# Kernel optimization log

Measured on AMD Instinct MI355X. Metric: run time of the kernel, lower is better.

## Reference

```python
import jax, jax.numpy as jnp
import numpy as np

N, E, D, ED, K = 16384, 524288, 64, 64, 16


def _lrelu(x, s):
    return jnp.where(x >= 0, x, s * x)


def _bn(x, g, b):
    # BatchNorm1d in training mode: biased batch statistics, eps=1e-5
    m = jnp.mean(x, axis=0)
    v = jnp.var(x, axis=0)
    return g * (x - m) * jax.lax.rsqrt(v + 1e-5) + b


def _segmax(msg, dst, n):
    # PyG aggr='max'; empty segments -> 0
    out = jax.ops.segment_max(msg, dst, num_segments=n)
    return jnp.where(jnp.isneginf(out), 0.0, out)


def _knn(x, k):
    # cosine kNN with self loops (bt_cosine=True, bt_self_loop=True)
    n = x.shape[0]
    xn = x * jax.lax.rsqrt(jnp.sum(x * x, axis=1, keepdims=True) + 1e-12)
    sim = jnp.where(jnp.eye(n, dtype=bool), -jnp.inf, xn @ xn.T)  # [n,n]
    idx = jax.lax.top_k(sim, k)[1]  # [n,k] sources j per target i
    loops = jnp.arange(n)
    src = jnp.concatenate([idx.reshape(-1), loops])
    dst = jnp.concatenate([jnp.repeat(loops, k), loops])
    return src, dst


def _static(x, src, dst, ea, w1, w2, w3, wl, n):
    # message: cat(x_j - x_i, edge_attr); scatter-max; update MLP (LeakyReLU 0.1)
    msg = jnp.concatenate([x[src] - x[dst], ea], axis=1)
    h = _segmax(msg, dst, n)
    h = _lrelu(h @ w1, 0.1)
    h = _lrelu(h @ w2, 0.1)
    h = _lrelu(h @ w3, 0.1)
    return _lrelu(x @ wl, 0.1) + h


def _dynamic(x, k, m1, m2, wl, n):
    # kNN recomputed under no_grad each call
    src, dst = _knn(jax.lax.stop_gradient(x), k)
    xi = x[dst]
    m = jnp.concatenate([xi, x[src] - xi], axis=1)
    m = _lrelu(m @ m1, 0.2)
    m = _lrelu(m @ m2, 0.2)
    return _lrelu(x @ wl, 0.1) + _segmax(m, dst, n)


def setup_inputs() -> dict:
    key = jax.random.key(0)
    ks = jax.random.split(key, 32)
    def w(i, shape):
        return jax.random.normal(ks[i], shape, dtype=jnp.float32) * 0.05
    return {
        'node_embedding': w(0, (N, D)),
        'edge_embedding': w(1, (E, ED)),
        'edge_index': jax.random.randint(ks[2], (2, E), 0, N),
        'k': K,
        'sg1_w1': w(3, (128, 96)), 'sg1_w2': w(4, (96, 64)), 'sg1_w3': w(5, (64, 64)), 'sg1_lin': w(6, (64, 64)),
        'sg2_w1': w(7, (128, 128)), 'sg2_w2': w(8, (128, 128)), 'sg2_w3': w(9, (128, 128)), 'sg2_lin': w(10, (64, 128)),
        'sg3_w1': w(11, (192, 192)), 'sg3_w2': w(12, (192, 192)), 'sg3_w3': w(13, (192, 192)), 'sg3_lin': w(14, (128, 192)),
        'dg1_m1': w(15, (128, 128)), 'dg1_m2': w(16, (128, 128)), 'dg1_lin': w(17, (64, 128)),
        'dg2_m1': w(18, (256, 192)), 'dg2_m2': w(19, (192, 192)), 'dg2_lin': w(20, (128, 192)),
        'f1_w': w(21, (704, 1024)), 'f1_g': jnp.ones(1024, jnp.float32), 'f1_b': jnp.zeros(1024, jnp.float32),
        'f2_w1': w(22, (1728, 512)), 'f2_g1': jnp.ones(512, jnp.float32), 'f2_b1': jnp.zeros(512, jnp.float32),
        'f2_w2': w(23, (512, 256)), 'f2_g2': jnp.ones(256, jnp.float32), 'f2_b2': jnp.zeros(256, jnp.float32),
        'f2_w3': w(24, (256, 128)),
    }


def reference(node_embedding, edge_embedding, edge_index, k,
              sg1_w1, sg1_w2, sg1_w3, sg1_lin,
              sg2_w1, sg2_w2, sg2_w3, sg2_lin,
              sg3_w1, sg3_w2, sg3_w3, sg3_lin,
              dg1_m1, dg1_m2, dg1_lin,
              dg2_m1, dg2_m2, dg2_lin,
              f1_w, f1_g, f1_b,
              f2_w1, f2_g1, f2_b1, f2_w2, f2_g2, f2_b2, f2_w3):
    n = node_embedding.shape[0]
    src, dst = edge_index[0], edge_index[1]
    sg1 = _static(node_embedding, src, dst, edge_embedding, sg1_w1, sg1_w2, sg1_w3, sg1_lin, n)
    sg2 = _static(sg1, src, dst, edge_embedding, sg2_w1, sg2_w2, sg2_w3, sg2_lin, n)
    sg3 = _static(sg2, src, dst, edge_embedding, sg3_w1, sg3_w2, sg3_w3, sg3_lin, n)
    dg1 = _dynamic(sg1, k, dg1_m1, dg1_m2, dg1_lin, n)
    dg2 = _dynamic(dg1, k, dg2_m1, dg2_m2, dg2_lin, n)
    cat1 = jnp.concatenate([sg1, dg1, dg2, sg2, sg3], axis=1)  # [N, 704]
    f1 = _lrelu(_bn(cat1 @ f1_w, f1_g, f1_b), 0.2)
    cat2 = jnp.concatenate([f1, cat1], axis=1)  # [N, 1728]
    h = _lrelu(_bn(cat2 @ f2_w1, f2_g1, f2_b1), 0.2)
    h = _lrelu(_bn(h @ f2_w2, f2_g2, f2_b2), 0.2)
    return h @ f2_w3  # [N, 128]
```

## Files before the change

### kernel.cpp

```cpp
#include <hip/hip_runtime.h>
#include <math.h>

typedef unsigned short u16;
typedef unsigned int u32;
typedef unsigned long long u64;
typedef __attribute__((ext_vector_type(8))) short short8v;
typedef __attribute__((ext_vector_type(4))) float f32x4;

static const int NN  = 16384;
static const int NE  = 524288;
static const int SCC = 1024;
static const int KEDGE = 17;

__device__ __forceinline__ u16 f2b(float v){
  u32 u = __float_as_uint(v);
  u += 0x7FFFu + ((u >> 16) & 1u);
  return (u16)(u >> 16);
}
__device__ __forceinline__ float b2f(u16 h){ return __uint_as_float(((u32)h) << 16); }

__device__ __forceinline__ void gl_lds16(const u16* g, u16* l){
  __builtin_amdgcn_global_load_lds(
      (const __attribute__((address_space(1))) u32*)(g),
      (__attribute__((address_space(3))) u32*)(l), 16, 0, 0);
}

__global__ void k_fill_i32(int* p, int v, int n){
  int i = blockIdx.x*256 + threadIdx.x; if (i < n) p[i] = v;
}
__global__ void k_split3(const float* __restrict__ s, u16* __restrict__ h,
                         u16* __restrict__ m, u16* __restrict__ l, int n,
                         int C, int ldo, int co, int ldl){
  int i = blockIdx.x*256 + threadIdx.x; if (i >= n) return;
  int r = i / C, c = i % C;
  float v = s[i];
  u16 hh = f2b(v);
  float rr = v - b2f(hh);
  u16 mm_ = f2b(rr);
  size_t o = (size_t)r*ldo + co + c;
  h[o] = hh; m[o] = mm_;
  if (l) l[(size_t)r*ldl + c] = f2b(rr - b2f(mm_));
}
__global__ void k_wprep3(const float* __restrict__ W, int K, int N, int Npad,
                         u16* __restrict__ h, u16* __restrict__ m, u16* __restrict__ l){
  int idx = blockIdx.x*256 + threadIdx.x; if (idx >= K*Npad) return;
  int n = idx / K, k = idx % K;
  float v = (n < N) ? W[(size_t)k*N + n] : 0.f;
  u16 hh = f2b(v); h[idx] = hh;
  float r = v - b2f(hh);
  u16 mm_ = f2b(r); m[idx] = mm_;
  l[idx] = f2b(r - b2f(mm_));
}

__global__ void k_hist(const int* __restrict__ dst, int* __restrict__ cnt){
  int e = blockIdx.x*256 + threadIdx.x; if (e < NE) atomicAdd(&cnt[dst[e]], 1);
}
__global__ void k_scan(const int* __restrict__ cnt, int* __restrict__ off){
  __shared__ int part[1024];
  int t = threadIdx.x;
  int base = t*16;
  int loc[16]; int s = 0;
#pragma unroll
  for (int q=0;q<16;q++){ loc[q] = s; s += cnt[base+q]; }
  part[t] = s; __syncthreads();
  for (int d=1; d<1024; d<<=1){
    int v = (t>=d) ? part[t-d] : 0; __syncthreads();
    part[t] += v; __syncthreads();
  }
  int prev = (t==0) ? 0 : part[t-1];
#pragma unroll
  for (int q=0;q<16;q++) off[base+q] = prev + loc[q];
  if (t == 1023) off[NN] = part[1023];
}
__global__ void k_csr_fill(const int* __restrict__ src, const int* __restrict__ dst,
                           const int* __restrict__ off, int* __restrict__ cur,
                           int* __restrict__ csrc, int* __restrict__ ceid){
  int e = blockIdx.x*256 + threadIdx.x; if (e >= NE) return;
  int d = dst[e];
  int p = atomicAdd(&cur[d], 1);
  int idx = off[d] + p;
  csrc[idx] = src[e];
  ceid[idx] = e;
}

__global__ void k_static_segmax(const float* __restrict__ x, int Dx,
                                const float* __restrict__ ea,
                                const int* __restrict__ off,
                                const int* __restrict__ csrc,
                                const int* __restrict__ ceid,
                                u16* __restrict__ th, u16* __restrict__ tm,
                                u16* __restrict__ tl){
  int i = blockIdx.x, c = threadIdx.x;
  int DM = Dx + 64;
  int s = off[i], e = off[i+1];
  float mx = -INFINITY;
  float v;
  if (c < Dx){
    for (int t = s; t < e; t++) mx = fmaxf(mx, x[(size_t)csrc[t]*Dx + c]);
    v = (s == e) ? 0.f : (mx - x[(size_t)i*Dx + c]);
  } else {
    int cc = c - Dx;
    for (int t = s; t < e; t++) mx = fmaxf(mx, ea[(size_t)ceid[t]*64 + cc]);
    v = (s == e) ? 0.f : mx;
  }
  size_t o = (size_t)i*DM + c;
  u16 h = f2b(v); th[o] = h;
  float r = v - b2f(h);
  u16 mm_ = f2b(r); tm[o] = mm_;
  tl[o] = f2b(r - b2f(mm_));
}

template<int P, int GATHER>
__global__ __launch_bounds__(256) void k_mgemm(
    const u16* __restrict__ Ah, const u16* __restrict__ Am, const u16* __restrict__ Al,
    int lda, int ldal,
    const u16* __restrict__ Bh, const u16* __restrict__ Bm, const u16* __restrict__ Bl,
    int ldb,
    float* __restrict__ Cf, u16* __restrict__ Ch, u16* __restrict__ Cm, u16* __restrict__ Cl,
    int ldc, int ldsp, int cosp, int ldspl,
    int K, int Nc, float slope, int flags, int colbase,
    const float* __restrict__ Xf, const int* __restrict__ topig, int c0g, int Dxg)
{
  constexpr int NC = (P == 3) ? 3 : 2;
  __shared__ u16 lds[NC*2*4096];
  const int t = threadIdx.x;
  const int m0 = blockIdx.y * 128, n0 = blockIdx.x * 128;
  const int wave = t >> 6, lane = t & 63;
  const int wr = (wave >> 1) << 6, wc = (wave & 1) << 6;
  const int l15 = lane & 15, l4 = lane >> 4;
  f32x4 acc[4][4] = {};

  const u16* Ap[3] = {Ah, Am, Al};
  const int ldav[3] = {lda, lda, ldal};
  const u16* Bp[3] = {Bh, Bm, Bl};

  const int c0c = wave*128 + lane, c1c = c0c + 64;
  const int r0c = c0c & 127, s0c = c0c >> 7;
  const int r1c = c1c & 127, s1c = c1c >> 7;
  const int lb0 = (wave*128)*8;
  const int lb1 = (wave*128 + 64)*8;

  size_t gA0[3], gA1[3], gB0[3], gB1[3];
#pragma unroll
  for (int cc=0; cc<NC; cc++){
    if (!GATHER){
      gA0[cc] = (size_t)(m0 + r0c)*ldav[cc] + s0c*8;
      gA1[cc] = (size_t)(m0 + r1c)*ldav[cc] + s1c*8;
    }
    gB0[cc] = (size_t)(n0 + r0c)*ldb + s0c*8;
    gB1[cc] = (size_t)(n0 + r1c)*ldb + s1c*8;
  }

  const int sr = t & 127, sseg = t >> 7;
  int node_i = 0, node_j = 0;
  if (GATHER){
    int erow = m0 + sr;
    int i = c0g + erow / KEDGE;
    int slot = erow % KEDGE;
    node_i = i;
    node_j = (slot < 16) ? topig[i*16 + slot] : i;
  }

  for (int k0 = 0; k0 < K; k0 += 32){
    __attribute__((aligned(16))) u16 hb[16], mb[16], lcb[16];
    if (GATHER){
      int kpos = k0 + sseg*16;
      bool side = kpos < Dxg;
      int kk = side ? kpos : kpos - Dxg;
      const float* xi = Xf + (size_t)node_i*Dxg + kk;
      const float* xj = Xf + (size_t)node_j*Dxg + kk;
#pragma unroll
      for (int q4=0;q4<4;q4++){
        float4 a = *(const float4*)(xi + q4*4);
        if (!side){
          float4 b = *(const float4*)(xj + q4*4);
          a = make_float4(b.x-a.x, b.y-a.y, b.z-a.z, b.w-a.w);
        }
        float vv[4] = {a.x, a.y, a.z, a.w};
#pragma unroll
        for (int q=0;q<4;q++){
          float v = vv[q];
          u16 h = f2b(v); hb[q4*4+q] = h;
          float r = v - b2f(h);
          u16 mm_ = f2b(r); mb[q4*4+q] = mm_;
          if (NC == 3) lcb[q4*4+q] = f2b(r - b2f(mm_));
        }
      }
    }
    __syncthreads();
    if (GATHER){
      int base0 = (sseg*2)*1024 + sr*8;
      int base1 = (sseg*2+1)*1024 + sr*8;
      *(int4*)&lds[0*4096 + base0] = *(const int4*)&hb[0];
      *(int4*)&lds[0*4096 + base1] = *(const int4*)&hb[8];
      *(int4*)&lds[1*4096 + base0] = *(const int4*)&mb[0];
      *(int4*)&lds[1*4096 + base1] = *(const int4*)&mb[8];
      if (NC == 3){
        *(int4*)&lds[2*4096 + base0] = *(const int4*)&lcb[0];
        *(int4*)&lds[2*4096 + base1] = *(const int4*)&lcb[8];
      }
    } else {
#pragma unroll
      for (int cc=0; cc<NC; cc++){
        gl_lds16(Ap[cc] + gA0[cc] + k0, &lds[cc*4096 + lb0]);
        gl_lds16(Ap[cc] + gA1[cc] + k0, &lds[cc*4096 + lb1]);
      }
    }
#pragma unroll
    for (int cc=0; cc<NC; cc++){
      gl_lds16(Bp[cc] + gB0[cc] + k0, &lds[(NC+cc)*4096 + lb0]);
      gl_lds16(Bp[cc] + gB1[cc] + k0, &lds[(NC+cc)*4096 + lb1]);
    }
    __syncthreads();
    short8v fa[NC][4], fb[NC][4];
#pragma unroll
    for (int m=0;m<4;m++){
      int ra = l4*1024 + (wr + m*16 + l15)*8;
      int rb = l4*1024 + (wc + m*16 + l15)*8;
#pragma unroll
      for (int cc=0;cc<NC;cc++){
        fa[cc][m] = *(const short8v*)&lds[cc*4096 + ra];
        fb[cc][m] = *(const short8v*)&lds[(NC+cc)*4096 + rb];
      }
    }
#pragma unroll
    for (int m=0;m<4;m++)
#pragma unroll
      for (int n=0;n<4;n++){
        if (P == 3){
          acc[m][n] = __builtin_amdgcn_mfma_f32_16x16x32_bf16(fa[1][m], fb[1][n], acc[m][n], 0,0,0);
          acc[m][n] = __builtin_amdgcn_mfma_f32_16x16x32_bf16(fa[0][m], fb[2][n], acc[m][n], 0,0,0);
          acc[m][n] = __builtin_amdgcn_mfma_f32_16x16x32_bf16(fa[2][m], fb[0][n], acc[m][n], 0,0,0);
        }
        acc[m][n] = __builtin_amdgcn_mfma_f32_16x16x32_bf16(fa[0][m], fb[1][n], acc[m][n], 0,0,0);
        acc[m][n] = __builtin_amdgcn_mfma_f32_16x16x32_bf16(fa[1][m], fb[0][n], acc[m][n], 0,0,0);
        acc[m][n] = __builtin_amdgcn_mfma_f32_16x16x32_bf16(fa[0][m], fb[0][n], acc[m][n], 0,0,0);
      }
  }

  const float NEG = -__builtin_inff();
#pragma unroll
  for (int n=0;n<4;n++){
    int col0 = n0 + wc + n*16;
    if (col0 >= Nc) continue;
    int col = col0 + l15;
#pragma unroll
    for (int m=0;m<4;m++){
      int rowb = m0 + wr + m*16 + l4*4;
#pragma unroll
      for (int r=0;r<4;r++){
        int row = rowb + r;
        float v = acc[m][n][r];
        if ((flags & 2) && row == colbase + col) v = NEG;
        else v = (v >= 0.f) ? v : v*slope;
        if (col < Nc){
          if (flags & 1) v += Cf[(size_t)row*ldc + col];
          if (Cf) Cf[(size_t)row*ldc + col] = v;
          if (Ch){
            size_t o = (size_t)row*ldsp + cosp + col;
            u16 h = f2b(v); Ch[o] = h;
            float rr = v - b2f(h);
            u16 mm_ = f2b(rr); Cm[o] = mm_;
            if (Cl) Cl[(size_t)row*ldspl + col] = f2b(rr - b2f(mm_));
          }
        }
      }
    }
  }
}

__global__ void k_normalize(const float* __restrict__ x,
                            u16* __restrict__ oh, u16* __restrict__ om,
                            u16* __restrict__ ol, int Dx){
  int i = blockIdx.x, lane = threadIdx.x;
  size_t o0 = (size_t)i*Dx + lane;
  float a = x[o0];
  float b = 0.f;
  if (Dx == 128) b = x[o0 + 64];
  float ss = a*a + b*b;
  for (int d = 32; d; d >>= 1) ss += __shfl_xor(ss, d);
  float rs = rsqrtf(ss + 1e-12f);
  float va = a*rs;
  u16 h = f2b(va); oh[o0] = h;
  float r = va - b2f(h);
  u16 mm_ = f2b(r); om[o0] = mm_;
  ol[o0] = f2b(r - b2f(mm_));
  if (Dx == 128){
    float vb = b*rs;
    u16 h2 = f2b(vb); oh[o0+64] = h2;
    float r2 = vb - b2f(h2);
    u16 m2 = f2b(r2); om[o0+64] = m2;
    ol[o0+64] = f2b(r2 - b2f(m2));
  }
}

__global__ void k_topk_merge(const float* __restrict__ S, int colbase,
                             float* __restrict__ topv, int* __restrict__ topi,
                             int first){
  const float INF = __builtin_inff();
  int i = blockIdx.x*4 + (threadIdx.x >> 6);
  int lane = threadIdx.x & 63;
  const float* row = S + (size_t)i * SCC;

  float4 va = *(const float4*)(row + 0*256 + lane*4);
  float4 vb = *(const float4*)(row + 1*256 + lane*4);
  float4 vc = *(const float4*)(row + 2*256 + lane*4);
  float4 vd = *(const float4*)(row + 3*256 + lane*4);
  float cv[16]; int cj[16];
  {
    float t0[4]={va.x,va.y,va.z,va.w}, t1[4]={vb.x,vb.y,vb.z,vb.w},
          t2[4]={vc.x,vc.y,vc.z,vc.w}, t3[4]={vd.x,vd.y,vd.z,vd.w};
#pragma unroll
    for (int q=0;q<4;q++){
      cv[q]    = t0[q]; cj[q]    = colbase + 0*256 + lane*4 + q;
      cv[4+q]  = t1[q]; cj[4+q]  = colbase + 1*256 + lane*4 + q;
      cv[8+q]  = t2[q]; cj[8+q]  = colbase + 2*256 + lane*4 + q;
      cv[12+q] = t3[q]; cj[12+q] = colbase + 3*256 + lane*4 + q;
    }
#pragma unroll
    for (int q=0;q<16;q++) if (cj[q] == i) cv[q] = -INF;
  }

  float pv = -INF; int pj = 0x7fffffff;
  if (!first){
    if (lane < 16){ pv = topv[i*16+lane]; pj = topi[i*16+lane]; }
    float tv = __shfl(pv, 15); int tj = __shfl(pj, 15);
    int cnt = 0;
#pragma unroll
    for (int q=0;q<16;q++){
      bool s = (cv[q] > tv) || (cv[q] == tv && cj[q] < tj);
      cnt += __popcll(__ballot(s));
    }
    if (cnt == 0) return;
    if (cnt <= 24){
#pragma unroll
      for (int q=0;q<16;q++){
        bool s = (cv[q] > tv) || (cv[q] == tv && cj[q] < tj);
        u64 msk = __ballot(s);
        while (msk){
          int src = __ffsll((long long)msk) - 1; msk &= msk - 1;
          float v = __shfl(cv[q], src);
          int   j = __shfl(cj[q], src);
          if ((v > tv) || (v == tv && j < tj)){
            bool eb = (pv > v) || (pv == v && pj < j);
            u32 mb = (u32)__ballot(eb) & 0xFFFFu;
            int p = __popc(mb);
            float sv = __shfl_up(pv, 1); int sj = __shfl_up(pj, 1);
            if (lane < 16 && lane >= p){
              if (lane == p){ pv = v; pj = j; }
              else          { pv = sv; pj = sj; }
            }
            tv = __shfl(pv, 15); tj = __shfl(pj, 15);
          }
        }
      }
      if (lane < 16){ topv[i*16+lane] = pv; topi[i*16+lane] = pj; }
      return;
    }
  }

  float myv = -INF; int myj = 0x7fffffff;
#pragma unroll
  for (int r=0;r<16;r++){
    float lv = pv; int lj = pj;
#pragma unroll
    for (int q=0;q<16;q++){
      if ((cv[q] > lv) || (cv[q] == lv && cj[q] < lj)){ lv = cv[q]; lj = cj[q]; }
    }
    float bv = lv; int bj = lj;
    for (int d=32; d; d>>=1){
      float ov = __shfl_xor(bv, d); int oj = __shfl_xor(bj, d);
      if ((ov > bv) || (ov == bv && oj < bj)){ bv = ov; bj = oj; }
    }
    if (lj == bj){
      if (pj == bj) pv = -INF;
      else {
#pragma unroll
        for (int q=0;q<16;q++) if (cj[q] == bj) cv[q] = -INF;
      }
    }
    if (lane == r){ myv = bv; myj = bj; }
  }
  if (lane < 16){ topv[i*16+lane] = myv; topi[i*16+lane] = myj; }
}

__global__ void k_segmax_add(const float* __restrict__ mo, int H2, int c0,
                             float* __restrict__ outp){
  int ii = blockIdx.x;
  int c = threadIdx.x;
  float m = -INFINITY;
  for (int s=0;s<KEDGE;s++) m = fmaxf(m, mo[(size_t)(ii*KEDGE+s)*H2 + c]);
  outp[(size_t)(c0+ii)*H2 + c] += m;
}

__global__ void k_bn_part(const float* __restrict__ X, int C,
                          float* __restrict__ psum, float* __restrict__ psq){
  int c = blockIdx.x*64 + (threadIdx.x & 63);
  int rl = threadIdx.x >> 6;
  int r0 = blockIdx.y * 512;
  float s = 0.f, q = 0.f;
  for (int r = r0 + rl; r < r0 + 512; r += 4){
    float v = X[(size_t)r*C + c];
    s += v; q += v*v;
  }
  __shared__ float ls[256], lq[256];
  ls[threadIdx.x] = s; lq[threadIdx.x] = q;
  __syncthreads();
  if (rl == 0){
    int tt = threadIdx.x;
    psum[blockIdx.y*C + c] = ls[tt] + ls[tt+64] + ls[tt+128] + ls[tt+192];
    psq [blockIdx.y*C + c] = lq[tt] + lq[tt+64] + lq[tt+128] + lq[tt+192];
  }
}
__global__ void k_bn_stats(const float* __restrict__ psum, const float* __restrict__ psq,
                           int C, float* __restrict__ stat){
  int c = blockIdx.x*256 + threadIdx.x; if (c >= C) return;
  float s = 0.f, q = 0.f;
  for (int ch=0; ch<32; ch++){ s += psum[ch*C + c]; q += psq[ch*C + c]; }
  float m = s * (1.f/16384.f);
  float var = q * (1.f/16384.f) - m*m;
  stat[c] = m;
  stat[C + c] = rsqrtf(var + 1e-5f);
}
__global__ void k_bn_apply(const float* __restrict__ X, int Cshift, int C,
                           const float* __restrict__ stat,
                           const float* __restrict__ g, const float* __restrict__ b,
                           u16* __restrict__ Oh, u16* __restrict__ Om,
                           int ldo, int co, int total){
  for (int idx = blockIdx.x*256 + threadIdx.x; idx < total; idx += gridDim.x*256){
    int c = idx & (C-1);
    int r = idx >> Cshift;
    float v = (X[idx] - stat[c]) * stat[C + c] * g[c] + b[c];
    v = (v >= 0.f) ? v : 0.2f*v;
    size_t o = (size_t)r*ldo + co + c;
    u16 h = f2b(v); Oh[o] = h;
    Om[o] = f2b(v - b2f(h));
  }
}

extern "C" void kernel_launch(void* const* d_in, const int* in_sizes, int n_in,
                              void* d_out, int out_size, void* d_ws, size_t ws_size,
                              hipStream_t stream) {
  (void)in_sizes; (void)n_in; (void)out_size; (void)ws_size;
  const float* x0   = (const float*)d_in[0];
  const float* ea   = (const float*)d_in[1];
  const int*   ei   = (const int*)d_in[2];
  const float* f1_g = (const float*)d_in[23];
  const float* f1_b = (const float*)d_in[24];
  const float* f2_g1= (const float*)d_in[26];
  const float* f2_b1= (const float*)d_in[27];
  const float* f2_g2= (const float*)d_in[29];
  const float* f2_b2= (const float*)d_in[30];
  float* out = (float*)d_out;

  const float* wsrc[22] = {
    (const float*)d_in[4],(const float*)d_in[5],(const float*)d_in[6],(const float*)d_in[7],
    (const float*)d_in[8],(const float*)d_in[9],(const float*)d_in[10],(const float*)d_in[11],
    (const float*)d_in[12],(const float*)d_in[13],(const float*)d_in[14],(const float*)d_in[15],
    (const float*)d_in[16],(const float*)d_in[17],(const float*)d_in[18],
    (const float*)d_in[19],(const float*)d_in[20],(const float*)d_in[21],
    (const float*)d_in[22],(const float*)d_in[25],(const float*)d_in[28],(const float*)d_in[31]
  };
  const int wK[22] = {128,96,64,64, 128,128,128,64, 192,192,192,128,
                      128,128,64, 256,192,128, 704, 1728, 512, 256};
  const int wN[22] = {96,64,64,64, 128,128,128,128, 192,192,192,192,
                      128,128,128, 192,192,192, 1024, 512, 256, 128};
  int wNp[22];
  for (int i=0;i<22;i++) wNp[i] = (wN[i] + 127) & ~127;

  char* w = (char*)d_ws;
  size_t off = 0;
  auto alloc = [&](size_t bytes)->char*{
    char* p = w + off; off = (off + bytes + 255) & ~(size_t)255; return p;
  };
  float* sg1f = (float*)alloc((size_t)NN*64*4);
  float* sg2f = (float*)alloc((size_t)NN*128*4);
  float* dg1f = (float*)alloc((size_t)NN*128*4);
  u16* cat1h = (u16*)alloc((size_t)NN*704*2);
  u16* cat1m = (u16*)alloc((size_t)NN*704*2);
  u16* sg1l  = (u16*)alloc((size_t)NN*64*2);
  u16* dg1l  = (u16*)alloc((size_t)NN*128*2);
  float* bnp  = (float*)alloc((size_t)2*32*1024*4);
  float* bns  = (float*)alloc((size_t)2*1024*4);
  u16 *wh[22], *wm[22], *wl[22];
  for (int i=0;i<22;i++){
    size_t e = (size_t)wK[i]*wNp[i];
    wh[i] = (u16*)alloc(e*2); wm[i] = (u16*)alloc(e*2); wl[i] = (u16*)alloc(e*2);
  }
  char* arena = alloc((size_t)120*1024*1024);
  size_t ac = 0;
  auto aalloc = [&](size_t b)->char*{
    char* p = arena + ac; ac = (ac + b + 255) & ~(size_t)255; return p;
  };

  auto MG = [&](int P, const u16* Ah, const u16* Am, const u16* Al, int lda, int ldal,
                const u16* Bh, const u16* Bm, const u16* Bl, int ldb,
                float* Cf, u16* Ch, u16* Cm, u16* Cl, int ldc, int ldsp, int cosp, int ldspl,
                int M, int K, int Nc, float slope, int flags, int colbase){
    dim3 g((Nc+127)/128, M/128);
    if (P == 3)
      k_mgemm<3,0><<<g,256,0,stream>>>(Ah,Am,Al,lda,ldal,Bh,Bm,Bl,ldb,
        Cf,Ch,Cm,Cl,ldc,ldsp,cosp,ldspl,K,Nc,slope,flags,colbase,nullptr,nullptr,0,0);
    else
      k_mgemm<2,0><<<g,256,0,stream>>>(Ah,Am,Al,lda,ldal,Bh,Bm,Bl,ldb,
        Cf,Ch,Cm,Cl,ldc,ldsp,cosp,ldspl,K,Nc,slope,flags,colbase,nullptr,nullptr,0,0);
  };
  auto MGG = [&](int P, const float* Xf, const int* topig, int c0g, int Dxg,
                 const u16* Bh, const u16* Bm, const u16* Bl, int ldb,
                 u16* Ch, u16* Cm, u16* Cl, int ldsp, int ldspl,
                 int M, int Nc, float slope){
    dim3 g((Nc+127)/128, M/128);
    if (P == 3)
      k_mgemm<3,1><<<g,256,0,stream>>>(nullptr,nullptr,nullptr,0,0,Bh,Bm,Bl,ldb,
        nullptr,Ch,Cm,Cl,0,ldsp,0,ldspl,2*Dxg,Nc,slope,0,0,Xf,topig,c0g,Dxg);
    else
      k_mgemm<2,1><<<g,256,0,stream>>>(nullptr,nullptr,nullptr,0,0,Bh,Bm,Bl,ldb,
        nullptr,Ch,Cm,Cl,0,ldsp,0,ldspl,2*Dxg,Nc,slope,0,0,Xf,topig,c0g,Dxg);
  };

  for (int i=0;i<22;i++){
    int e = wK[i]*wNp[i];
    k_wprep3<<<(e+255)/256, 256, 0, stream>>>(wsrc[i], wK[i], wN[i], wNp[i], wh[i], wm[i], wl[i]);
  }

  ac = 0;
  u16* t1s[3]; for (int c=0;c<3;c++) t1s[c] = (u16*)aalloc((size_t)NN*192*2);
  u16* t2s[3]; for (int c=0;c<3;c++) t2s[c] = (u16*)aalloc((size_t)NN*192*2);
  float* sof32 = (float*)aalloc((size_t)NN*192*4);
  int* csr_cnt = (int*)aalloc((size_t)NN*4);
  int* csr_off = (int*)aalloc((size_t)(NN+1)*4);
  int* csr_src = (int*)aalloc((size_t)NE*4);
  int* csr_eid = (int*)aalloc((size_t)NE*4);
  u16* x0s[3]; for (int c=0;c<3;c++) x0s[c] = (u16*)aalloc((size_t)NN*64*2);

  k_split3<<<(NN*64+255)/256, 256, 0, stream>>>(x0, x0s[0], x0s[1], x0s[2], NN*64, 64, 64, 0, 64);

  const int* srcp = ei;
  const int* dstp = ei + NE;
  k_fill_i32<<<(NN+255)/256, 256, 0, stream>>>(csr_cnt, 0, NN);
  k_hist<<<NE/256, 256, 0, stream>>>(dstp, csr_cnt);
  k_scan<<<1, 1024, 0, stream>>>(csr_cnt, csr_off);
  k_fill_i32<<<(NN+255)/256, 256, 0, stream>>>(csr_cnt, 0, NN);
  k_csr_fill<<<NE/256, 256, 0, stream>>>(srcp, dstp, csr_off, csr_cnt, csr_src, csr_eid);

  auto static_layer = [&](int P, const float* xf,
                          const u16* xh, const u16* xm, const u16* xl, int lda, int ldal,
                          int Dx, int wi, float* of, int co, u16* lout, int H1, int H2){
    int DM = Dx + 64;
    k_static_segmax<<<NN, DM, 0, stream>>>(xf, Dx, ea, csr_off, csr_src, csr_eid,
                                           t1s[0], t1s[1], t1s[2]);
    MG(P, t1s[0],t1s[1],t1s[2], DM,DM, wh[wi],wm[wi],wl[wi], DM,
       nullptr, t2s[0],t2s[1],t2s[2], 0, H1,0,H1, NN, DM, H1, 0.1f, 0, 0);
    MG(P, t2s[0],t2s[1],t2s[2], H1,H1, wh[wi+1],wm[wi+1],wl[wi+1], H1,
       nullptr, t1s[0],t1s[1],t1s[2], 0, H2,0,H2, NN, H1, H2, 0.1f, 0, 0);
    MG(P, xh,xm,xl, lda,ldal, wh[wi+3],wm[wi+3],wl[wi+3], Dx,
       of, nullptr,nullptr,nullptr, H2,0,0,0, NN, Dx, H2, 0.1f, 0, 0);
    MG(P, t1s[0],t1s[1],t1s[2], H2,H2, wh[wi+2],wm[wi+2],wl[wi+2], H2,
       of, cat1h,cat1m,lout, H2, 704,co,(lout? (co==0?64:128) : 0),
       NN, H2, H2, 0.1f, 1, 0);
  };
  static_layer(3, x0,  x0s[0],x0s[1],x0s[2], 64,64, 64, 0, sg1f, 0,   sg1l, 96, 64);
  static_layer(2, sg1f, cat1h+0,  cat1m+0,  nullptr, 704,0, 64, 4, sg2f, 384, nullptr, 128, 128);
  static_layer(2, sg2f, cat1h+384,cat1m+384,nullptr, 704,0, 128,8, sof32,512, nullptr, 192, 192);

  ac = 0;
  u16* xns[3]; for (int c=0;c<3;c++) xns[c] = (u16*)aalloc((size_t)NN*128*2);
  float* topv = (float*)aalloc((size_t)NN*16*4);
  int*   topi = (int*)aalloc((size_t)NN*16*4);
  float* dg2of = (float*)aalloc((size_t)NN*192*4);
  size_t dyn0 = ac;

  auto dyn_layer = [&](int P, const float* xf,
                       const u16* xh, const u16* xm, const u16* xl, int lda, int ldal,
                       int Dx, int wi, float* ofp, int co, u16* lout, int H1, int H2, int nch){
    const int R = nch*KEDGE;
    ac = dyn0;
    float* S = (float*)aalloc((size_t)NN*SCC*4);
    ac = dyn0;
    u16* mms[3]; for (int c=0;c<3;c++) mms[c] = (u16*)aalloc((size_t)R*H1*2);
    float* mout = (float*)aalloc((size_t)R*H2*4);

    k_normalize<<<NN, 64, 0, stream>>>(xf, xns[0], xns[1], xns[2], Dx);
    for (int cb = 0; cb < NN; cb += SCC){
      MG(3, xns[0],xns[1],xns[2], Dx,Dx,
         xns[0]+(size_t)cb*Dx, xns[1]+(size_t)cb*Dx, xns[2]+(size_t)cb*Dx, Dx,
         S, nullptr,nullptr,nullptr, SCC,0,0,0, NN, Dx, SCC, 1.0f, 2, cb);
      k_topk_merge<<<NN/4, 256, 0, stream>>>(S, cb, topv, topi, cb == 0);
    }
    MG(P, xh,xm,xl, lda,ldal, wh[wi+2],wm[wi+2],wl[wi+2], Dx,
       ofp, nullptr,nullptr,nullptr, H2,0,0,0, NN, Dx, H2, 0.1f, 0, 0);
    for (int c0 = 0; c0 < NN; c0 += nch){
      MGG(P, xf, topi, c0, Dx, wh[wi],wm[wi],wl[wi], 2*Dx,
          mms[0],mms[1],(P==3?mms[2]:nullptr), H1,H1, R, H1, 0.2f);
      MG(P, mms[0],mms[1],mms[2], H1,H1, wh[wi+1],wm[wi+1],wl[wi+1], H1,
         mout, nullptr,nullptr,nullptr, H2,0,0,0, R, H1, H2, 0.2f, 0, 0);
      k_segmax_add<<<nch, H2, 0, stream>>>(mout, H2, c0, ofp);
    }
    k_split3<<<(NN*H2+255)/256, 256, 0, stream>>>(ofp, cat1h, cat1m, lout,
                                                  NN*H2, H2, 704, co, H2);
  };
  dyn_layer(3, sg1f, cat1h+0, cat1m+0, sg1l, 704,64, 64,  12, dg1f, 64,  dg1l, 128, 128, 4096);
  dyn_layer(2, dg1f, cat1h+64,cat1m+64,nullptr,704,0, 128, 15, dg2of,192, nullptr,192, 192, 2048);

  ac = 0;
  u16*   f1sh = (u16*)aalloc((size_t)NN*1024*2);
  u16*   f1sm = (u16*)aalloc((size_t)NN*1024*2);
  float* fscr = (float*)aalloc((size_t)NN*512*4);
  u16* h2h = f1sh;
  u16* h2m = f1sm;
  float* h3f32 = (float*)(f1sm + (size_t)NN*512);
  u16* h3h = f1sh + (size_t)NN*512;
  u16* h3m = h3h + (size_t)NN*256;

  auto bn = [&](const float* X, int C, int Cshift, const float* g, const float* b,
                u16* Oh, u16* Om, int ldo, int co){
    k_bn_part<<<dim3(C/64, 32), 256, 0, stream>>>(X, C, bnp, bnp + 32*1024);
    k_bn_stats<<<(C+255)/256, 256, 0, stream>>>(bnp, bnp + 32*1024, C, bns);
    k_bn_apply<<<2048, 256, 0, stream>>>(X, Cshift, C, bns, g, b, Oh, Om, ldo, co, NN*C);
  };

  for (int p = 0; p < 2; p++){
    MG(2, cat1h,cat1m,nullptr, 704,0, wh[18]+(size_t)p*512*704, wm[18]+(size_t)p*512*704, nullptr, 704,
       fscr, nullptr,nullptr,nullptr, 512,0,0,0, NN, 704, 512, 1.f, 0, 0);
    bn(fscr, 512, 9, f1_g + p*512, f1_b + p*512, f1sh, f1sm, 1024, p*512);
  }
  MG(2, f1sh,f1sm,nullptr, 1024,0, wh[19],wm[19],nullptr, 1728,
     fscr, nullptr,nullptr,nullptr, 512,0,0,0, NN, 1024, 512, 1.f, 0, 0);
  MG(2, cat1h,cat1m,nullptr, 704,0, wh[19]+1024,wm[19]+1024,nullptr, 1728,
     fscr, nullptr,nullptr,nullptr, 512,0,0,0, NN, 704, 512, 1.f, 1, 0);
  bn(fscr, 512, 9, f2_g1, f2_b1, h2h, h2m, 512, 0);
  MG(2, h2h,h2m,nullptr, 512,0, wh[20],wm[20],nullptr, 512,
     h3f32, nullptr,nullptr,nullptr, 256,0,0,0, NN, 512, 256, 1.f, 0, 0);
  bn(h3f32, 256, 8, f2_g2, f2_b2, h3h, h3m, 256, 0);
  MG(2, h3h,h3m,nullptr, 256,0, wh[21],wm[21],nullptr, 256,
     out, nullptr,nullptr,nullptr, 128,0,0,0, NN, 256, 128, 1.f, 0, 0);
}
```

Baseline: 4.607 ms.

## Swizzle GEMM workgroup order and drop incremental top-k fast path

The GEMM kernel remaps its linear block id so that consecutive workgroups are spread across eight groups, changing which output tiles run together and aiming for better cache locality or XCD distribution. The kNN top-k merge kernel drops its early-exit and insertion fast path for later column chunks and always runs the full 16-round selection. The second change removes the cheap exit used when a chunk holds no better candidates, so it likely adds work. The swizzle also assumes the total block count is divisible by eight.

```diff
diff --git a/kernel.cpp b/kernel.cpp
--- a/kernel.cpp
+++ b/kernel.cpp
@@ -124,7 +124,11 @@
   constexpr int NC = (P == 3) ? 3 : 2;
   __shared__ u16 lds[NC*2*4096];
   const int t = threadIdx.x;
-  const int m0 = blockIdx.y * 128, n0 = blockIdx.x * 128;
+  const int nwgx = gridDim.x;
+  const int bid = blockIdx.y * nwgx + blockIdx.x;
+  const int cpx = (nwgx * gridDim.y) >> 3;
+  const int swz = (bid & 7) * cpx + (bid >> 3);
+  const int m0 = (swz / nwgx) * 128, n0 = (swz % nwgx) * 128;
   const int wave = t >> 6, lane = t & 63;
   const int wr = (wave >> 1) << 6, wc = (wave & 1) << 6;
   const int l15 = lane & 15, l4 = lane >> 4;
@@ -322,42 +326,7 @@
   }
 
   float pv = -INF; int pj = 0x7fffffff;
-  if (!first){
-    if (lane < 16){ pv = topv[i*16+lane]; pj = topi[i*16+lane]; }
-    float tv = __shfl(pv, 15); int tj = __shfl(pj, 15);
-    int cnt = 0;
-#pragma unroll
-    for (int q=0;q<16;q++){
-      bool s = (cv[q] > tv) || (cv[q] == tv && cj[q] < tj);
-      cnt += __popcll(__ballot(s));
-    }
-    if (cnt == 0) return;
-    if (cnt <= 24){
-#pragma unroll
-      for (int q=0;q<16;q++){
-        bool s = (cv[q] > tv) || (cv[q] == tv && cj[q] < tj);
-        u64 msk = __ballot(s);
-        while (msk){
-          int src = __ffsll((long long)msk) - 1; msk &= msk - 1;
-          float v = __shfl(cv[q], src);
-          int   j = __shfl(cj[q], src);
-          if ((v > tv) || (v == tv && j < tj)){
-            bool eb = (pv > v) || (pv == v && pj < j);
-            u32 mb = (u32)__ballot(eb) & 0xFFFFu;
-            int p = __popc(mb);
-            float sv = __shfl_up(pv, 1); int sj = __shfl_up(pj, 1);
-            if (lane < 16 && lane >= p){
-              if (lane == p){ pv = v; pj = j; }
-              else          { pv = sv; pj = sj; }
-            }
-            tv = __shfl(pv, 15); tj = __shfl(pj, 15);
-          }
-        }
-      }
-      if (lane < 16){ topv[i*16+lane] = pv; topi[i*16+lane] = pj; }
-      return;
-    }
-  }
+  if (!first && lane < 16){ pv = topv[i*16+lane]; pj = topi[i*16+lane]; }
 
   float myv = -INF; int myj = 0x7fffffff;
 #pragma unroll
```

Measured after the change: 6.409 ms. 1.39x slower.
